# Performance work log

Measured on AMD Instinct MI355X. Metric: run time of the kernel, lower is better.

Reference implementation:

```python
import jax, jax.numpy as jnp
import numpy as np

B, C, H, W = 16, 2, 768, 768
WIN = 5                      # window_size: maxima kernel AND gauss-fit window
PAD = WIN // 2
HEATMAP_AXIS = 1
THRESHOLD = 0.5
MAX_DET = 393216             # fixed-size pad for data-dependent nonzero()


def setup_inputs() -> dict:
    key = jax.random.key(0)
    # strictly positive heat so log(z) in Guo's fit is well-defined
    x = jax.random.uniform(key, (B, C, H, W), dtype=jnp.float32, minval=1e-4, maxval=1.0)
    return {"x": x}


def _forward(x):
    heat = x[:, HEATMAP_AXIS]                                   # [B,H,W]
    th = jnp.where(heat > THRESHOLD, heat, 0.0)
    # kornia dilation with ones kernel (center zeroed) == max over neighbors excl. center
    padded = jnp.pad(th, ((0, 0), (PAD, PAD), (PAD, PAD)), constant_values=-np.inf)
    dilated = jnp.full(th.shape, -np.inf, th.dtype)
    for dy in range(WIN):
        for dx in range(WIN):
            if dy == PAD and dx == PAD:
                continue
            dilated = jnp.maximum(dilated, padded[:, dy:dy + H, dx:dx + W])
    local_max = (th > dilated).reshape(-1)                      # strict local maxima above threshold
    (flat_idx,) = jnp.nonzero(local_max, size=MAX_DET, fill_value=0)  # row-major, like torch.nonzero
    valid = jnp.arange(MAX_DET) < local_max.sum()
    bidx = flat_idx // (H * W)
    rc = flat_idx % (H * W)
    r = rc // W
    cc = rc % W
    sub = jnp.linspace((-WIN) // 2 + 1, WIN // 2, WIN)
    xs, ys = jnp.meshgrid(sub, sub, indexing='xy')              # xs varies along columns
    xf = xs.reshape(-1).astype(jnp.float32)                     # [K]
    yf = ys.reshape(-1).astype(jnp.float32)
    off = jnp.arange(WIN) - PAD
    off_r = jnp.repeat(off, WIN)                                # row-major window flattening
    off_c = jnp.tile(off, WIN)
    rows = jnp.clip(r[:, None] + off_r[None, :], 0, H - 1)      # clamp at borders
    cols = jnp.clip(cc[:, None] + off_c[None, :], 0, W - 1)
    z = heat[bidx[:, None], rows, cols]                         # [N,K] window intensities
    z = jnp.clip(z, 1e-6, None)                                 # numerical guard for log
    xb = jnp.broadcast_to(xf, z.shape)
    yb = jnp.broadcast_to(yf, z.shape)
    # quadratic basis [1, x, x^2, y, xy, y^2]
    basis = jnp.stack([jnp.ones_like(xb), xb, xb * xb, yb, xb * yb, yb * yb], -1)  # [N,K,6]
    wgt = z * z                                                  # Guo's weights
    Aw = basis * wgt[:, :, None]
    bvec = jnp.log(z) * wgt
    ATA = jnp.einsum('nki,nkj->nij', Aw, Aw)                     # [N,6,6]
    ATb = jnp.einsum('nki,nk->ni', Aw, bvec)                     # [N,6]
    coef = jnp.einsum('nij,nj->ni', jnp.linalg.inv(ATA), ATb)    # [N,6]
    Aq, Bl, Cc = coef[:, [2, 5]], coef[:, [1, 3]], coef[:, [0, 4]]
    good = valid & jnp.all(Aq < 0, axis=-1)                      # concave fit -> real sigma
    g = good[:, None]
    Aq_s = jnp.where(g, Aq, -0.5)                                # guard against NaN at padded slots
    sigma = jnp.sqrt(-1.0 / (2.0 * Aq_s))
    mu = Bl * sigma ** 2
    height = jnp.exp(jnp.where(g, Cc + 0.5 * mu ** 2 / sigma ** 2, 0.0))
    pos = jnp.stack([r, cc], -1).astype(jnp.float32) + mu[:, ::-1]  # maxima_indices + mu[:,[1,0]]
    sigma = jnp.where(g, sigma, 0.0)
    pos = jnp.where(g, pos, 0.0)
    height = jnp.where(g, height, 0.0)
    return sigma, pos, height, good


def reference(x):
    return _forward(x)
```

## Files before the change

kernel.cpp:

```cpp
#include <hip/hip_runtime.h>
#include <hip/hip_bf16.h>
#include <cstdint>

#define BATCH 16
#define HDIM 768
#define WDIM 768
#define HW (HDIM * WDIM)
#define NPIX (BATCH * HW)
#define MAX_DET 393216

#define TILE_R 16
#define NTILES (BATCH * (HDIM / TILE_R))
#define WORDS_PER_TILE 192
#define LDS_ROWS 20
#define LDS_C 776
#define VEC_PER_ROW 194
#define TOT_VEC (LDS_ROWS * VEC_PER_ROW)
#define NTHREADS 384

#define WORD_OFF 0u
#define CNT_OFF  1179648u
#define TOT_OFF  1182720u
#define IDX_OFF  1183744u

#define SIGMA_BASE 0
#define POS_BASE   786432
#define HGT_BASE   1572864
#define GOOD_BASE  2359296

__device__ __forceinline__ float fast_logf(float zf) {
    int ib = __float_as_int(zf);
    int e = ((ib >> 23) & 255) - 127;
    float m1 = __int_as_float((ib & 0x007fffff) | 0x3f800000);
    float lg = __builtin_amdgcn_logf(m1);
    return ((float)e + lg) * 0.69314718055994531f;
}

__device__ __forceinline__ double fast_rcp(double d) {
    double r = (double)__builtin_amdgcn_rcpf((float)d);
    r = r * (2.0 - d * r);
    r = r * (2.0 - d * r);
    return r;
}

__global__ __launch_bounds__(NTHREADS) void maskcount_kernel(const float* __restrict__ x,
                                                             unsigned long long* __restrict__ words,
                                                             int* __restrict__ counts) {
    __shared__ float lds[LDS_ROWS * LDS_C];
    const int tid  = threadIdx.x;
    const int tile = blockIdx.x;
    const int b  = tile / 48;
    const int rt = tile - b * 48;
    const int r0 = rt * TILE_R;
    const float* heat = x + (size_t)b * (2 * HW) + HW;

    for (int i = tid; i < TOT_VEC; i += NTHREADS) {
        int lr = (unsigned)i / VEC_PER_ROW;
        int q  = i - lr * VEC_PER_ROW;
        int row = r0 - 2 + lr;
        int col = 4 * q - 4;
        float4 v = make_float4(0.f, 0.f, 0.f, 0.f);
        if (row >= 0 && row < HDIM && col >= 0 && col <= WDIM - 4) {
            v = *reinterpret_cast<const float4*>(heat + (size_t)row * WDIM + col);
        }
        float4 t;
        t.x = v.x > 0.5f ? v.x : 0.f;
        t.y = v.y > 0.5f ? v.y : 0.f;
        t.z = v.z > 0.5f ? v.z : 0.f;
        t.w = v.w > 0.5f ? v.w : 0.f;
        *reinterpret_cast<float4*>(&lds[lr * LDS_C + 4 * q]) = t;
    }
    __syncthreads();

    const int wv   = tid >> 6;
    const int lane = tid & 63;
    const int h    = wv / 3;
    const int st   = wv - 3 * h;
    const int lrow0 = h * 8;

    auto readrow = [&](int ldsrow, float* h5, float* hx, float* tc) {
        const float* p = &lds[ldsrow * LDS_C + st * 256 + 4 * lane];
        float4 a = *reinterpret_cast<const float4*>(p);
        float4 bb = *reinterpret_cast<const float4*>(p + 4);
        float4 cc = *reinterpret_cast<const float4*>(p + 8);
        float t2=a.z,t3=a.w,t4=bb.x,t5=bb.y,t6=bb.z,t7=bb.w,t8=cc.x,t9=cc.y;
        float pp0=fmaxf(t2,t3), pp1=fmaxf(t3,t4), pp2=fmaxf(t4,t5), pp3=fmaxf(t5,t6),
              pp4=fmaxf(t6,t7), pp5=fmaxf(t7,t8), pp6=fmaxf(t8,t9);
        h5[0]=fmaxf(fmaxf(pp0,pp2),t6);  hx[0]=fmaxf(pp0,pp3);  tc[0]=t4;
        h5[1]=fmaxf(fmaxf(pp1,pp3),t7);  hx[1]=fmaxf(pp1,pp4);  tc[1]=t5;
        h5[2]=fmaxf(fmaxf(pp2,pp4),t8);  hx[2]=fmaxf(pp2,pp5);  tc[2]=t6;
        h5[3]=fmaxf(fmaxf(pp3,pp5),t9);  hx[3]=fmaxf(pp3,pp6);  tc[3]=t7;
    };

    float h5r[5][4], hxr[5][4], tcr[5][4];
    #pragma unroll
    for (int j = 0; j < 4; ++j)
        readrow(lrow0 + j, h5r[j], hxr[j], tcr[j]);

    unsigned nibword = 0;
    #pragma unroll
    for (int k = 0; k < 8; ++k) {
        readrow(lrow0 + k + 4, h5r[(k+4)%5], hxr[(k+4)%5], tcr[(k+4)%5]);
        unsigned nib = 0;
        #pragma unroll
        for (int c = 0; c < 4; ++c) {
            float dil = fmaxf(fmaxf(h5r[k%5][c], h5r[(k+1)%5][c]),
                        fmaxf(hxr[(k+2)%5][c],
                        fmaxf(h5r[(k+3)%5][c], h5r[(k+4)%5][c])));
            if (tcr[(k+2)%5][c] > dil) nib |= (1u << c);
        }
        nibword |= nib << (4 * k);
    }

    __syncthreads();
    unsigned* lu = (unsigned*)lds;
    int* su = (int*)lds + 512;
    lu[tid] = nibword;
    __syncthreads();

    int pc = 0;
    if (tid < WORDS_PER_TILE) {
        const int r   = tid / 12;
        const int c12 = tid - r * 12;
        const int s2  = c12 >> 2;
        const int wi  = c12 & 3;
        const int h2  = r >> 3;
        const int k2  = r & 7;
        const int wv2 = h2 * 3 + s2;
        const int sft = 4 * k2;
        const uint4* p = (const uint4*)&lu[wv2 * 64 + wi * 16];
        uint4 q0 = p[0], q1 = p[1], q2 = p[2], q3 = p[3];
        unsigned lo = 0, hi = 0;
        lo |= ((q0.x >> sft) & 0xFu) << 0;   lo |= ((q0.y >> sft) & 0xFu) << 4;
        lo |= ((q0.z >> sft) & 0xFu) << 8;   lo |= ((q0.w >> sft) & 0xFu) << 12;
        lo |= ((q1.x >> sft) & 0xFu) << 16;  lo |= ((q1.y >> sft) & 0xFu) << 20;
        lo |= ((q1.z >> sft) & 0xFu) << 24;  lo |= ((q1.w >> sft) & 0xFu) << 28;
        hi |= ((q2.x >> sft) & 0xFu) << 0;   hi |= ((q2.y >> sft) & 0xFu) << 4;
        hi |= ((q2.z >> sft) & 0xFu) << 8;   hi |= ((q2.w >> sft) & 0xFu) << 12;
        hi |= ((q3.x >> sft) & 0xFu) << 16;  hi |= ((q3.y >> sft) & 0xFu) << 20;
        hi |= ((q3.z >> sft) & 0xFu) << 24;  hi |= ((q3.w >> sft) & 0xFu) << 28;
        unsigned long long word = (unsigned long long)lo |
                                  ((unsigned long long)hi << 32);
        words[tile * WORDS_PER_TILE + tid] = word;
        pc = __popcll(word);
    }
    if (tid < 256) su[tid] = (tid < WORDS_PER_TILE) ? pc : 0;
    __syncthreads();
    for (int off = 128; off > 0; off >>= 1) {
        if (tid < off) su[tid] += su[tid + off];
        __syncthreads();
    }
    if (tid == 0) counts[tile] = su[0];
}

__global__ __launch_bounds__(192) void scatter_kernel(const unsigned long long* __restrict__ words,
                                                      const int* __restrict__ counts,
                                                      int* __restrict__ flat_idx,
                                                      int* __restrict__ total) {
    __shared__ int s[256];
    __shared__ int s2[WORDS_PER_TILE];
    __shared__ int blockoff;
    const int t = threadIdx.x;
    const int tile = blockIdx.x;

    int acc = 0;
    for (int i = t; i < tile; i += 192) acc += counts[i];
    s[t] = acc;
    if (t < 64) s[192 + t] = 0;
    __syncthreads();
    for (int off = 128; off > 0; off >>= 1) {
        if (t < off) s[t] += s[t + off];
        __syncthreads();
    }
    if (t == 0) blockoff = s[0];
    __syncthreads();

    unsigned long long m = words[tile * WORDS_PER_TILE + t];
    int pc = __popcll(m);
    s2[t] = pc;
    __syncthreads();
    for (int off = 1; off < WORDS_PER_TILE; off <<= 1) {
        int add = (t >= off) ? s2[t - off] : 0;
        __syncthreads();
        s2[t] += add;
        __syncthreads();
    }
    if (tile == NTILES - 1 && t == WORDS_PER_TILE - 1)
        *total = blockoff + s2[t];

    int base = blockoff + s2[t] - pc;
    int idx0 = (tile * WORDS_PER_TILE + t) << 6;
    while (m) {
        int j = __builtin_ctzll(m);
        if (base < MAX_DET) flat_idx[base] = idx0 + j;
        ++base;
        m &= m - 1;
    }
}

__global__ __launch_bounds__(256) void fit_kernel(const float* __restrict__ x,
                                                  const int* __restrict__ flat_idx,
                                                  const int* __restrict__ total,
                                                  float* __restrict__ out) {
    int n = blockIdx.x * 256 + threadIdx.x;
    int count = min(*total, MAX_DET);
    float sx = 0.f, sy = 0.f, p0 = 0.f, p1 = 0.f, h0 = 0.f, h1 = 0.f, goodf = 0.f;
    if (n < count) {
        int idx = flat_idx[n];
        int b = idx / HW;
        int rc = idx - b * HW;
        int r = rc / WDIM;
        int c = rc - r * WDIM;
        const float* heat = x + (size_t)b * (2 * HW) + HW;

        float zv[25];
        #pragma unroll
        for (int dy = 0; dy < 5; ++dy) {
            int rr = min(max(r + dy - 2, 0), HDIM - 1);
            const float* hp = heat + (size_t)rr * WDIM;
            #pragma unroll
            for (int dx = 0; dx < 5; ++dx) {
                int cc = min(max(c + dx - 2, 0), WDIM - 1);
                zv[dy * 5 + dx] = hp[cc];
            }
        }

        float M00=0,M10=0,M01=0,M20=0,M11=0,M02=0,M30=0,M21=0,M12=0,M03=0;
        float M40=0,M31=0,M22=0,M13=0,M04=0;
        float N0=0,N1=0,N2=0,N3=0,N4=0,N5=0;
        #pragma unroll
        for (int dy = -2; dy <= 2; ++dy) {
            float S0=0,S1=0,S2=0,S3=0,S4=0,T0=0,T1=0,T2=0;
            #pragma unroll
            for (int dx = -2; dx <= 2; ++dx) {
                float zf = fmaxf(zv[(dy + 2) * 5 + dx + 2], 1e-6f);
                float z2 = zf * zf;
                float w2 = z2 * z2;
                float wl = w2 * fast_logf(zf);
                const float X = (float)dx;
                S0 += w2; T0 += wl;
                if (dx != 0) {
                    S1 += w2 * X;
                    S2 += w2 * (X * X);
                    S3 += w2 * (X * X * X);
                    S4 += w2 * (X * X * X * X);
                    T1 += wl * X;
                    T2 += wl * (X * X);
                }
            }
            const float Y = (float)dy;
            M00 += S0; M10 += S1; M20 += S2; M30 += S3; M40 += S4;
            N0 += T0; N1 += T1; N2 += T2;
            if (dy != 0) {
                float Y2 = Y * Y, Y3 = Y2 * Y, Y4 = Y2 * Y2;
                M01 += S0 * Y;  M11 += S1 * Y;  M21 += S2 * Y;  M31 += S3 * Y;
                M02 += S0 * Y2; M12 += S1 * Y2; M22 += S2 * Y2;
                M03 += S0 * Y3; M13 += S1 * Y3;
                M04 += S0 * Y4;
                N3 += T0 * Y; N4 += T1 * Y; N5 += T0 * Y2;
            }
        }

        double A[6][7];
        A[0][0]=M00; A[0][1]=M10; A[0][2]=M20; A[0][3]=M01; A[0][4]=M11; A[0][5]=M02; A[0][6]=N0;
        A[1][0]=M10; A[1][1]=M20; A[1][2]=M30; A[1][3]=M11; A[1][4]=M21; A[1][5]=M12; A[1][6]=N1;
        A[2][0]=M20; A[2][1]=M30; A[2][2]=M40; A[2][3]=M21; A[2][4]=M31; A[2][5]=M22; A[2][6]=N2;
        A[3][0]=M01; A[3][1]=M11; A[3][2]=M21; A[3][3]=M02; A[3][4]=M12; A[3][5]=M03; A[3][6]=N3;
        A[4][0]=M11; A[4][1]=M21; A[4][2]=M31; A[4][3]=M12; A[4][4]=M22; A[4][5]=M13; A[4][6]=N4;
        A[5][0]=M02; A[5][1]=M12; A[5][2]=M22; A[5][3]=M03; A[5][4]=M13; A[5][5]=M04; A[5][6]=N5;

        #pragma unroll
        for (int i = 0; i < 6; ++i) {
            double inv = fast_rcp(A[i][i]);
            #pragma unroll
            for (int j = i + 1; j < 7; ++j) A[i][j] *= inv;
            #pragma unroll
            for (int ii = i + 1; ii < 6; ++ii) {
                double f = A[ii][i];
                #pragma unroll
                for (int j = i + 1; j < 7; ++j) A[ii][j] -= f * A[i][j];
            }
        }
        double cv[6];
        #pragma unroll
        for (int i = 5; i >= 0; --i) {
            double v = A[i][6];
            #pragma unroll
            for (int j = i + 1; j < 6; ++j) v -= A[i][j] * cv[j];
            cv[i] = v;
        }

        double aqx = cv[2], aqy = cv[5];
        if (aqx < 0.0 && aqy < 0.0) {
            double sx2 = -0.5 * fast_rcp(aqx);
            double sy2 = -0.5 * fast_rcp(aqy);
            sx2 = fmin(sx2, 1e300);
            sy2 = fmin(sy2, 1e300);
            double sigx = sqrt(sx2), sigy = sqrt(sy2);
            double mux = cv[1] * sx2, muy = cv[3] * sy2;
            sx = (float)sigx;
            sy = (float)sigy;
            p0 = (float)((double)r + muy);
            p1 = (float)((double)c + mux);
            float a0 = (float)((cv[0] + 0.5 * cv[1] * cv[1] * sx2) * 1.4426950408889634);
            float a1 = (float)((cv[4] + 0.5 * cv[3] * cv[3] * sy2) * 1.4426950408889634);
            a0 = fminf(a0, 126.0f);
            a1 = fminf(a1, 126.0f);
            h0 = exp2f(a0);
            h1 = exp2f(a1);
            goodf = 1.0f;
        }
    }
    out[SIGMA_BASE + 2 * n]     = sx;
    out[SIGMA_BASE + 2 * n + 1] = sy;
    out[POS_BASE + 2 * n]       = p0;
    out[POS_BASE + 2 * n + 1]   = p1;
    out[HGT_BASE + 2 * n]       = h0;
    out[HGT_BASE + 2 * n + 1]   = h1;
    out[GOOD_BASE + n]          = goodf;
}

extern "C" void kernel_launch(void* const* d_in, const int* in_sizes, int n_in,
                              void* d_out, int out_size, void* d_ws, size_t ws_size,
                              hipStream_t stream) {
    const float* x = (const float*)d_in[0];
    float* out = (float*)d_out;
    char* ws = (char*)d_ws;

    unsigned long long* words = (unsigned long long*)(ws + WORD_OFF);
    int* counts  = (int*)(ws + CNT_OFF);
    int* total   = (int*)(ws + TOT_OFF);
    int* flatidx = (int*)(ws + IDX_OFF);

    maskcount_kernel<<<NTILES, NTHREADS, 0, stream>>>(x, words, counts);
    scatter_kernel<<<NTILES, 192, 0, stream>>>(words, counts, flatidx, total);
    fit_kernel<<<MAX_DET / 256, 256, 0, stream>>>(x, flatidx, total, out);
}
```

Baseline: 51.53 us.

## Halve maskcount tile height, pair tiles in scatter, vectorize fit window loads

The mask/count kernel now covers 8 rows per tile with 192 threads and a 12-row LDS halo, which doubles the block count and lowers LDS use per block so occupancy can rise. The trade is more halo re-reading. The scatter kernel keeps 192 words per block by merging two of the new tiles, so it launches half as many blocks and sums the per-tile counts over twice as many entries. The fit kernel loads each interior 5-wide window row with two float4 loads plus a register shift instead of five scalar loads. That adds a branch on the alignment offset and keeps the scalar path for border columns.

```diff
diff --git a/kernel.cpp b/kernel.cpp
--- a/kernel.cpp
+++ b/kernel.cpp
@@ -9,19 +9,19 @@
 #define NPIX (BATCH * HW)
 #define MAX_DET 393216
 
-#define TILE_R 16
+#define TILE_R 8
 #define NTILES (BATCH * (HDIM / TILE_R))
-#define WORDS_PER_TILE 192
-#define LDS_ROWS 20
+#define WORDS_PER_TILE 96
+#define LDS_ROWS 12
 #define LDS_C 776
 #define VEC_PER_ROW 194
 #define TOT_VEC (LDS_ROWS * VEC_PER_ROW)
-#define NTHREADS 384
+#define NTHREADS 192
 
 #define WORD_OFF 0u
 #define CNT_OFF  1179648u
-#define TOT_OFF  1182720u
-#define IDX_OFF  1183744u
+#define TOT_OFF  1185792u
+#define IDX_OFF  1187840u
 
 #define SIGMA_BASE 0
 #define POS_BASE   786432
@@ -49,34 +49,35 @@
     __shared__ float lds[LDS_ROWS * LDS_C];
     const int tid  = threadIdx.x;
     const int tile = blockIdx.x;
-    const int b  = tile / 48;
-    const int rt = tile - b * 48;
+    const int b  = tile / 96;
+    const int rt = tile - b * 96;
     const int r0 = rt * TILE_R;
     const float* heat = x + (size_t)b * (2 * HW) + HW;
 
-    for (int i = tid; i < TOT_VEC; i += NTHREADS) {
-        int lr = (unsigned)i / VEC_PER_ROW;
-        int q  = i - lr * VEC_PER_ROW;
-        int row = r0 - 2 + lr;
-        int col = 4 * q - 4;
-        float4 v = make_float4(0.f, 0.f, 0.f, 0.f);
-        if (row >= 0 && row < HDIM && col >= 0 && col <= WDIM - 4) {
-            v = *reinterpret_cast<const float4*>(heat + (size_t)row * WDIM + col);
-        }
-        float4 t;
-        t.x = v.x > 0.5f ? v.x : 0.f;
-        t.y = v.y > 0.5f ? v.y : 0.f;
-        t.z = v.z > 0.5f ? v.z : 0.f;
-        t.w = v.w > 0.5f ? v.w : 0.f;
-        *reinterpret_cast<float4*>(&lds[lr * LDS_C + 4 * q]) = t;
-    }
-    __syncthreads();
-
-    const int wv   = tid >> 6;
+    #pragma unroll
+    for (int it = 0; it < 13; ++it) {
+        int i = it * NTHREADS + tid;
+        if (i < TOT_VEC) {
+            int lr = (unsigned)i / VEC_PER_ROW;
+            int q  = i - lr * VEC_PER_ROW;
+            int row = r0 - 2 + lr;
+            int col = 4 * q - 4;
+            float4 v = make_float4(0.f, 0.f, 0.f, 0.f);
+            if (row >= 0 && row < HDIM && col >= 0 && col <= WDIM - 4) {
+                v = *reinterpret_cast<const float4*>(heat + (size_t)row * WDIM + col);
+            }
+            float4 t;
+            t.x = v.x > 0.5f ? v.x : 0.f;
+            t.y = v.y > 0.5f ? v.y : 0.f;
+            t.z = v.z > 0.5f ? v.z : 0.f;
+            t.w = v.w > 0.5f ? v.w : 0.f;
+            *reinterpret_cast<float4*>(&lds[lr * LDS_C + 4 * q]) = t;
+        }
+    }
+    __syncthreads();
+
+    const int st   = tid >> 6;
     const int lane = tid & 63;
-    const int h    = wv / 3;
-    const int st   = wv - 3 * h;
-    const int lrow0 = h * 8;
 
     auto readrow = [&](int ldsrow, float* h5, float* hx, float* tc) {
         const float* p = &lds[ldsrow * LDS_C + st * 256 + 4 * lane];
@@ -95,12 +96,12 @@
     float h5r[5][4], hxr[5][4], tcr[5][4];
     #pragma unroll
     for (int j = 0; j < 4; ++j)
-        readrow(lrow0 + j, h5r[j], hxr[j], tcr[j]);
+        readrow(j, h5r[j], hxr[j], tcr[j]);
 
     unsigned nibword = 0;
     #pragma unroll
     for (int k = 0; k < 8; ++k) {
-        readrow(lrow0 + k + 4, h5r[(k+4)%5], hxr[(k+4)%5], tcr[(k+4)%5]);
+        readrow(k + 4, h5r[(k+4)%5], hxr[(k+4)%5], tcr[(k+4)%5]);
         unsigned nib = 0;
         #pragma unroll
         for (int c = 0; c < 4; ++c) {
@@ -114,21 +115,18 @@
 
     __syncthreads();
     unsigned* lu = (unsigned*)lds;
-    int* su = (int*)lds + 512;
+    int* su = (int*)lds + 256;
     lu[tid] = nibword;
     __syncthreads();
 
     int pc = 0;
     if (tid < WORDS_PER_TILE) {
-        const int r   = tid / 12;
-        const int c12 = tid - r * 12;
+        const int k2  = tid / 12;
+        const int c12 = tid - k2 * 12;
         const int s2  = c12 >> 2;
         const int wi  = c12 & 3;
-        const int h2  = r >> 3;
-        const int k2  = r & 7;
-        const int wv2 = h2 * 3 + s2;
         const int sft = 4 * k2;
-        const uint4* p = (const uint4*)&lu[wv2 * 64 + wi * 16];
+        const uint4* p = (const uint4*)&lu[s2 * 64 + wi * 16];
         uint4 q0 = p[0], q1 = p[1], q2 = p[2], q3 = p[3];
         unsigned lo = 0, hi = 0;
         lo |= ((q0.x >> sft) & 0xFu) << 0;   lo |= ((q0.y >> sft) & 0xFu) << 4;
@@ -144,9 +142,10 @@
         words[tile * WORDS_PER_TILE + tid] = word;
         pc = __popcll(word);
     }
-    if (tid < 256) su[tid] = (tid < WORDS_PER_TILE) ? pc : 0;
-    __syncthreads();
-    for (int off = 128; off > 0; off >>= 1) {
+    if (tid < 128) su[tid] = (tid < WORDS_PER_TILE) ? pc : 0;
+    __syncthreads();
+    #pragma unroll
+    for (int off = 64; off > 0; off >>= 1) {
         if (tid < off) su[tid] += su[tid + off];
         __syncthreads();
     }
@@ -158,16 +157,17 @@
                                                       int* __restrict__ flat_idx,
                                                       int* __restrict__ total) {
     __shared__ int s[256];
-    __shared__ int s2[WORDS_PER_TILE];
+    __shared__ int s2[192];
     __shared__ int blockoff;
     const int t = threadIdx.x;
-    const int tile = blockIdx.x;
+    const int blk = blockIdx.x;
 
     int acc = 0;
-    for (int i = t; i < tile; i += 192) acc += counts[i];
+    for (int i = t; i < 2 * blk; i += 192) acc += counts[i];
     s[t] = acc;
     if (t < 64) s[192 + t] = 0;
     __syncthreads();
+    #pragma unroll
     for (int off = 128; off > 0; off >>= 1) {
         if (t < off) s[t] += s[t + off];
         __syncthreads();
@@ -175,21 +175,21 @@
     if (t == 0) blockoff = s[0];
     __syncthreads();
 
-    unsigned long long m = words[tile * WORDS_PER_TILE + t];
+    unsigned long long m = words[blk * 192 + t];
     int pc = __popcll(m);
     s2[t] = pc;
     __syncthreads();
-    for (int off = 1; off < WORDS_PER_TILE; off <<= 1) {
+    for (int off = 1; off < 192; off <<= 1) {
         int add = (t >= off) ? s2[t - off] : 0;
         __syncthreads();
         s2[t] += add;
         __syncthreads();
     }
-    if (tile == NTILES - 1 && t == WORDS_PER_TILE - 1)
-        *total = blockoff + s2[t];
+    if (blk == 767 && t == 191)
+        *total = blockoff + s2[191];
 
     int base = blockoff + s2[t] - pc;
-    int idx0 = (tile * WORDS_PER_TILE + t) << 6;
+    int idx0 = (blk * 192 + t) << 6;
     while (m) {
         int j = __builtin_ctzll(m);
         if (base < MAX_DET) flat_idx[base] = idx0 + j;
@@ -214,14 +214,34 @@
         const float* heat = x + (size_t)b * (2 * HW) + HW;
 
         float zv[25];
-        #pragma unroll
-        for (int dy = 0; dy < 5; ++dy) {
-            int rr = min(max(r + dy - 2, 0), HDIM - 1);
-            const float* hp = heat + (size_t)rr * WDIM;
-            #pragma unroll
-            for (int dx = 0; dx < 5; ++dx) {
-                int cc = min(max(c + dx - 2, 0), WDIM - 1);
-                zv[dy * 5 + dx] = hp[cc];
+        if (c >= 2 && c <= WDIM - 3) {
+            const int a   = (c - 2) & ~3;
+            const int ofs = (c - 2) & 3;
+            #pragma unroll
+            for (int dy = 0; dy < 5; ++dy) {
+                int rr = min(max(r + dy - 2, 0), HDIM - 1);
+                const float* hp = heat + (size_t)rr * WDIM + a;
+                float4 u0 = *reinterpret_cast<const float4*>(hp);
+                float4 u1 = *reinterpret_cast<const float4*>(hp + 4);
+                float b0=u0.x, b1=u0.y, b2=u0.z, b3=u0.w;
+                float b4=u1.x, b5=u1.y, b6=u1.z, b7=u1.w;
+                float v0, v1, v2, v3, v4;
+                if (ofs == 0)      { v0=b0; v1=b1; v2=b2; v3=b3; v4=b4; }
+                else if (ofs == 1) { v0=b1; v1=b2; v2=b3; v3=b4; v4=b5; }
+                else if (ofs == 2) { v0=b2; v1=b3; v2=b4; v3=b5; v4=b6; }
+                else               { v0=b3; v1=b4; v2=b5; v3=b6; v4=b7; }
+                zv[dy*5+0]=v0; zv[dy*5+1]=v1; zv[dy*5+2]=v2; zv[dy*5+3]=v3; zv[dy*5+4]=v4;
+            }
+        } else {
+            #pragma unroll
+            for (int dy = 0; dy < 5; ++dy) {
+                int rr = min(max(r + dy - 2, 0), HDIM - 1);
+                const float* hp = heat + (size_t)rr * WDIM;
+                #pragma unroll
+                for (int dx = 0; dx < 5; ++dx) {
+                    int cc = min(max(c + dx - 2, 0), WDIM - 1);
+                    zv[dy * 5 + dx] = hp[cc];
+                }
             }
         }
 
@@ -333,6 +353,6 @@
     int* flatidx = (int*)(ws + IDX_OFF);
 
     maskcount_kernel<<<NTILES, NTHREADS, 0, stream>>>(x, words, counts);
-    scatter_kernel<<<NTILES, 192, 0, stream>>>(words, counts, flatidx, total);
+    scatter_kernel<<<NTILES / 2, 192, 0, stream>>>(words, counts, flatidx, total);
     fit_kernel<<<MAX_DET / 256, 256, 0, stream>>>(x, flatidx, total, out);
 }
```

Result: slower. 52.83 us (+2.5%).
